# Kernel optimization log

Hardware: AMD Instinct MI355X
Metric: run time of the kernel (lower is better)

The kernel has to match this reference:

```python
import jax, jax.numpy as jnp
import numpy as np

N_NODES = 100000
N_EDGES = 1600000
N_GRAPHS = 64
D = 128          # input_features == hidden_sf*model_dim == out_sf*output_channels
N_CLASSES = 10   # out_dim
N_LAYERS = 3


def setup_inputs() -> dict:
    key = jax.random.key(0)
    ks = jax.random.split(key, 8)
    x = jax.random.normal(ks[0], (N_NODES, D), dtype=jnp.float32)
    edge_index = jax.random.randint(ks[1], (2, N_EDGES), 0, N_NODES, dtype=jnp.int64)
    batch = jnp.sort(jax.random.randint(ks[2], (N_NODES,), 0, N_GRAPHS, dtype=jnp.int64))
    s = 1.0 / np.sqrt(D)
    # PyG GraphConv: out = lin_rel(aggr(x_j)) + lin_root(x); lin_root has no bias
    W_rel = jax.random.uniform(ks[3], (N_LAYERS, D, D), jnp.float32, -s, s)
    W_root = jax.random.uniform(ks[4], (N_LAYERS, D, D), jnp.float32, -s, s)
    b_rel = jax.random.uniform(ks[5], (N_LAYERS, D), jnp.float32, -s, s)
    W_fc = jax.random.uniform(ks[6], (D, N_CLASSES), jnp.float32, -s, s)
    b_fc = jax.random.uniform(ks[7], (N_CLASSES,), jnp.float32, -s, s)
    return dict(x=x, edge_index=edge_index, batch=batch,
                W_rel=W_rel, W_root=W_root, b_rel=b_rel, W_fc=W_fc, b_fc=b_fc)


def reference(x, edge_index, batch, W_rel, W_root, b_rel, W_fc, b_fc):
    src, dst = edge_index[0], edge_index[1]  # messages flow src -> dst
    for i in range(N_LAYERS):  # small fixed layer count
        agg = jax.ops.segment_sum(x[src], dst, num_segments=N_NODES)  # [N, D] gather+scatter-add
        x = agg @ W_rel[i] + b_rel[i] + x @ W_root[i]
    # global mean pool over graphs
    counts = jax.ops.segment_sum(jnp.ones((N_NODES,), x.dtype), batch, num_segments=N_GRAPHS)
    pooled = jax.ops.segment_sum(x, batch, num_segments=N_GRAPHS) / jnp.maximum(counts, 1.0)[:, None]
    logits = pooled @ W_fc + b_fc  # [N_GRAPHS, N_CLASSES]
    return jax.nn.log_softmax(logits, axis=1)
```

## Files before the change

### kernel.cpp

```cpp
#include <hip/hip_runtime.h>
#include <hip/hip_bf16.h>

#define D 128
#define NGRAPHS 64
#define NCLASSES 10
#define NB 800
#define CAP 3072
#define EPB 8192

typedef unsigned short u16;
typedef unsigned int u32;
typedef __attribute__((ext_vector_type(8))) short bf16x8;
typedef __attribute__((ext_vector_type(4))) float f32x4;

__device__ __forceinline__ u16 rne_bf16(float f) {
  u32 u = __float_as_uint(f);
  u += 0x7FFFu + ((u >> 16) & 1u);
  return (u16)(u >> 16);
}
__device__ __forceinline__ float bf_lo(u32 u) { return __uint_as_float(u << 16); }
__device__ __forceinline__ float bf_hi(u32 u) { return __uint_as_float(u & 0xFFFF0000u); }

__device__ __forceinline__ void gload_lds16(const void* g, void* l) {
  __builtin_amdgcn_global_load_lds(
      (const __attribute__((address_space(1))) void*)g,
      (__attribute__((address_space(3))) void*)l, 16, 0, 0);
}

__global__ __launch_bounds__(256) void k_cast0(const float* __restrict__ x,
                                               u16* __restrict__ xb, long long n8) {
  long long i = (long long)blockIdx.x * 256 + threadIdx.x;
  if (i >= n8) return;
  const float4* xp = reinterpret_cast<const float4*>(x) + i * 2;
  float4 a = xp[0], b = xp[1];
  u32 w0 = rne_bf16(a.x) | ((u32)rne_bf16(a.y) << 16);
  u32 w1 = rne_bf16(a.z) | ((u32)rne_bf16(a.w) << 16);
  u32 w2 = rne_bf16(b.x) | ((u32)rne_bf16(b.y) << 16);
  u32 w3 = rne_bf16(b.z) | ((u32)rne_bf16(b.w) << 16);
  reinterpret_cast<uint4*>(xb)[i] = make_uint4(w0, w1, w2, w3);
}

__global__ __launch_bounds__(256) void k_prep_wt(const float* __restrict__ W_rel,
                                                 const float* __restrict__ W_root,
                                                 u16* __restrict__ Wt) {
  int id = blockIdx.x * 256 + threadIdx.x;
  if (id >= 6 * D * D) return;
  int col = id & 127;
  int k = (id >> 7) & 127;
  int m = id >> 14;
  const float* src = (m < 3) ? (W_rel + (size_t)m * D * D) : (W_root + (size_t)(m - 3) * D * D);
  Wt[(size_t)m * D * D + col * D + k] = rne_bf16(src[k * D + col]);
}

__global__ __launch_bounds__(256) void k_bin(
    const int* __restrict__ src, const int* __restrict__ dst,
    int* __restrict__ gcnt, u32* __restrict__ ebuf, int n_edges, int nb) {
  __shared__ int lh[NB];
  int tid = threadIdx.x;
  int e0 = blockIdx.x * EPB;
  for (int b = tid; b < NB; b += 256) lh[b] = 0;
  __syncthreads();
  for (int i = tid; i < EPB; i += 256) {
    int e = e0 + i;
    if (e < n_edges) atomicAdd(&lh[dst[e] >> 7], 1);
  }
  __syncthreads();
  for (int b = tid; b < nb; b += 256) {
    int c = lh[b];
    lh[b] = (c > 0) ? (b * CAP + atomicAdd(&gcnt[b], c)) : 0;
  }
  __syncthreads();
  for (int i = tid; i < EPB; i += 256) {
    int e = e0 + i;
    if (e < n_edges) {
      int d = dst[e];
      int slot = atomicAdd(&lh[d >> 7], 1);
      ebuf[slot] = ((u32)(d & 127) << 20) | (u32)src[e];
    }
  }
}

__global__ __launch_bounds__(256) void k_sort(
    const u32* __restrict__ ebuf, const int* __restrict__ gcnt,
    u32* __restrict__ eidx, int* __restrict__ rowptr, int* __restrict__ deg,
    int n_nodes) {
  __shared__ u32 earr[CAP];
  __shared__ int lh[128], sc[128], lcur[128];
  int tid = threadIdx.x;
  int b = blockIdx.x;
  int cnt = gcnt[b];
  int base = b * CAP;
  for (int i = tid; i < cnt; i += 256) earr[i] = ebuf[base + i];
  if (tid < 128) lh[tid] = 0;
  __syncthreads();
  for (int i = tid; i < cnt; i += 256) atomicAdd(&lh[earr[i] >> 20], 1);
  __syncthreads();
  if (tid < 128) sc[tid] = lh[tid];
  __syncthreads();
  #pragma unroll
  for (int off = 1; off < 128; off <<= 1) {
    int v = (tid < 128 && tid >= off) ? sc[tid - off] : 0;
    __syncthreads();
    if (tid < 128) sc[tid] += v;
    __syncthreads();
  }
  if (tid < 128) {
    int excl = sc[tid] - lh[tid];
    int n = b * 128 + tid;
    if (n < n_nodes) { rowptr[n] = base + excl; deg[n] = lh[tid]; }
    lcur[tid] = excl;
  }
  __syncthreads();
  for (int i = tid; i < cnt; i += 256) {
    u32 e = earr[i];
    int slot = atomicAdd(&lcur[e >> 20], 1);
    eidx[base + slot] = e & 0xFFFFF;
  }
}

__global__ __launch_bounds__(256) void k_gather(
    const u16* __restrict__ xb, const int* __restrict__ rowptr,
    const int* __restrict__ deg, const u32* __restrict__ eidx,
    u16* __restrict__ aggb, int n_nodes) {
  int tid = threadIdx.x;
  int lane = tid & 63;
  int n = blockIdx.x * 4 + (tid >> 6);
  if (n >= n_nodes) return;
  int es = lane >> 4;
  int c = lane & 15;
  int beg = rowptr[n];
  int dn = deg[n];
  float a0 = 0, a1 = 0, a2 = 0, a3 = 0, a4 = 0, a5 = 0, a6 = 0, a7 = 0;
  int i = 0;
  for (; i + 8 <= dn; i += 8) {
    int s0 = (int)eidx[beg + i + es];
    int s1 = (int)eidx[beg + i + 4 + es];
    uint4 v0 = *(reinterpret_cast<const uint4*>(xb + (size_t)s0 * D) + c);
    uint4 v1 = *(reinterpret_cast<const uint4*>(xb + (size_t)s1 * D) + c);
    a0 += bf_lo(v0.x) + bf_lo(v1.x); a1 += bf_hi(v0.x) + bf_hi(v1.x);
    a2 += bf_lo(v0.y) + bf_lo(v1.y); a3 += bf_hi(v0.y) + bf_hi(v1.y);
    a4 += bf_lo(v0.z) + bf_lo(v1.z); a5 += bf_hi(v0.z) + bf_hi(v1.z);
    a6 += bf_lo(v0.w) + bf_lo(v1.w); a7 += bf_hi(v0.w) + bf_hi(v1.w);
  }
  for (; i < dn; i += 4) {
    bool p = (i + es) < dn;
    int s = p ? (int)eidx[beg + i + es] : 0;
    if (p) {
      uint4 v = *(reinterpret_cast<const uint4*>(xb + (size_t)s * D) + c);
      a0 += bf_lo(v.x); a1 += bf_hi(v.x);
      a2 += bf_lo(v.y); a3 += bf_hi(v.y);
      a4 += bf_lo(v.z); a5 += bf_hi(v.z);
      a6 += bf_lo(v.w); a7 += bf_hi(v.w);
    }
  }
  #pragma unroll
  for (int d = 16; d <= 32; d <<= 1) {
    a0 += __shfl_xor(a0, d); a1 += __shfl_xor(a1, d);
    a2 += __shfl_xor(a2, d); a3 += __shfl_xor(a3, d);
    a4 += __shfl_xor(a4, d); a5 += __shfl_xor(a5, d);
    a6 += __shfl_xor(a6, d); a7 += __shfl_xor(a7, d);
  }
  if (es == 0) {
    u32 w0 = rne_bf16(a0) | ((u32)rne_bf16(a1) << 16);
    u32 w1 = rne_bf16(a2) | ((u32)rne_bf16(a3) << 16);
    u32 w2 = rne_bf16(a4) | ((u32)rne_bf16(a5) << 16);
    u32 w3 = rne_bf16(a6) | ((u32)rne_bf16(a7) << 16);
    *(reinterpret_cast<uint4*>(aggb + (size_t)n * D) + c) = make_uint4(w0, w1, w2, w3);
  }
}

__global__ __launch_bounds__(256) void k_gemm_mfma(
    const u16* __restrict__ A1, const u16* __restrict__ A2,
    const u16* __restrict__ Wt1, const u16* __restrict__ Wt2,
    const float* __restrict__ bias, u16* __restrict__ outp, int M) {
  __shared__ __align__(16) u16 As[2][128 * 64];
  __shared__ __align__(16) u16 Ws[2][128 * 64];
  int tid = threadIdx.x;
  int wave = tid >> 6, lane = tid & 63;
  int g = lane >> 4, lr = lane & 15;
  int r0 = blockIdx.x * 128;
  int wr = wave * 32;

  f32x4 acc[2][8];
  #pragma unroll
  for (int fr = 0; fr < 2; fr++)
    #pragma unroll
    for (int fc = 0; fc < 8; fc++)
      acc[fr][fc] = (f32x4){0.f, 0.f, 0.f, 0.f};

  const u16* Am[2] = {A1, A2};
  const u16* Wm[2] = {Wt1, Wt2};

  auto STAGE = [&](int buf, const u16* A, const u16* Wt, int kh) {
    #pragma unroll
    for (int i = 0; i < 4; i++) {
      int gI = i * 256 + tid;
      int row = gI >> 3;
      int cs = (gI & 7) ^ (row & 7);
      int rg = r0 + row; if (rg >= M) rg = M - 1;
      u16* la = &As[buf][(size_t)(i * 256 + wave * 64) * 8];
      gload_lds16(A + (size_t)rg * D + kh * 64 + cs * 8, la);
      u16* lw = &Ws[buf][(size_t)(i * 256 + wave * 64) * 8];
      gload_lds16(Wt + (size_t)row * D + kh * 64 + cs * 8, lw);
    }
  };

  STAGE(0, A1, Wt1, 0);
  __syncthreads();

  #pragma unroll 1
  for (int s = 0; s < 4; s++) {
    if (s < 3) {
      int ns = s + 1;
      STAGE(ns & 1, Am[ns >> 1], Wm[ns >> 1], ns & 1);
    }
    int buf = s & 1;
    #pragma unroll
    for (int kc = 0; kc < 2; kc++) {
      int kbyte = kc * 64 + g * 16;
      bf16x8 af[2];
      #pragma unroll
      for (int fr = 0; fr < 2; fr++) {
        int row = wr + fr * 16 + lr;
        int ob = (kbyte ^ ((row & 7) << 4)) >> 1;
        af[fr] = *reinterpret_cast<const bf16x8*>(&As[buf][row * 64 + ob]);
      }
      #pragma unroll
      for (int fc = 0; fc < 8; fc++) {
        int colw = fc * 16 + lr;
        int ob = (kbyte ^ ((colw & 7) << 4)) >> 1;
        bf16x8 bfv = *reinterpret_cast<const bf16x8*>(&Ws[buf][colw * 64 + ob]);
        #pragma unroll
        for (int fr = 0; fr < 2; fr++)
          acc[fr][fc] = __builtin_amdgcn_mfma_f32_16x16x32_bf16(
              af[fr], bfv, acc[fr][fc], 0, 0, 0);
      }
    }
    __syncthreads();
  }

  #pragma unroll
  for (int fc = 0; fc < 8; fc++) {
    float bc = bias[fc * 16 + lr];
    #pragma unroll
    for (int fr = 0; fr < 2; fr++) {
      #pragma unroll
      for (int j = 0; j < 4; j++) {
        int R = r0 + wr + fr * 16 + g * 4 + j;
        if (R < M)
          outp[(size_t)R * D + fc * 16 + lr] = rne_bf16(acc[fr][fc][j] + bc);
      }
    }
  }
}

#define CHUNK 256
__global__ __launch_bounds__(256) void k_pool(
    const u16* __restrict__ xb, const int* __restrict__ batch,
    float* __restrict__ pooled, int n_nodes) {
  int col = threadIdx.x & 127;
  int sub = threadIdx.x >> 7;
  int n0 = blockIdx.x * CHUNK;
  int nend = min(n0 + CHUNK, n_nodes);
  float sum = 0.f; int cur = -1;
  for (int n = n0 + sub; n < nend; n += 2) {
    int g = batch[n];
    if (g != cur) {
      if (cur >= 0) atomicAdd(&pooled[cur * D + col], sum);
      sum = 0.f; cur = g;
    }
    sum += __uint_as_float((u32)xb[(size_t)n * D + col] << 16);
  }
  if (cur >= 0) atomicAdd(&pooled[cur * D + col], sum);
}

__global__ __launch_bounds__(256) void k_bounds(
    const int* __restrict__ batch, int* __restrict__ start, int n) {
  int i = blockIdx.x * 256 + threadIdx.x;
  if (i >= n) return;
  int g = batch[i];
  if (i == 0 || batch[i - 1] != g) start[g] = i;
}

__global__ void k_head(const float* __restrict__ pooled, const int* __restrict__ gstart,
                       const float* __restrict__ W_fc, const float* __restrict__ b_fc,
                       float* __restrict__ outp, int n_nodes) {
  int g = threadIdx.x;
  if (g >= NGRAPHS) return;
  int s = gstart[g];
  int c = 0;
  if (s >= 0) {
    int e = n_nodes;
    for (int h = g + 1; h < NGRAPHS; h++)
      if (gstart[h] >= 0) { e = gstart[h]; break; }
    c = e - s;
  }
  float inv = 1.0f / fmaxf((float)c, 1.0f);
  float logits[NCLASSES];
  #pragma unroll
  for (int j = 0; j < NCLASSES; j++) logits[j] = b_fc[j];
  for (int k = 0; k < D; k++) {
    float p = pooled[g * D + k] * inv;
    #pragma unroll
    for (int j = 0; j < NCLASSES; j++) logits[j] += p * W_fc[k * NCLASSES + j];
  }
  float m = logits[0];
  #pragma unroll
  for (int j = 1; j < NCLASSES; j++) m = fmaxf(m, logits[j]);
  float s2 = 0.f;
  #pragma unroll
  for (int j = 0; j < NCLASSES; j++) s2 += expf(logits[j] - m);
  float lse = m + logf(s2);
  #pragma unroll
  for (int j = 0; j < NCLASSES; j++) outp[g * NCLASSES + j] = logits[j] - lse;
}

extern "C" void kernel_launch(void* const* d_in, const int* in_sizes, int n_in,
                              void* d_out, int out_size, void* d_ws, size_t ws_size,
                              hipStream_t stream) {
  const float* x      = (const float*)d_in[0];
  const int*   ei     = (const int*)d_in[1];
  const int*   batch  = (const int*)d_in[2];
  const float* W_rel  = (const float*)d_in[3];
  const float* W_root = (const float*)d_in[4];
  const float* b_rel  = (const float*)d_in[5];
  const float* W_fc   = (const float*)d_in[6];
  const float* b_fc   = (const float*)d_in[7];
  float* outp = (float*)d_out;

  int n_nodes = in_sizes[0] / D;
  int n_edges = in_sizes[1] / 2;
  const int* src = ei;
  const int* dst = ei + n_edges;
  int nb = (n_nodes + 127) / 128;

  char* ws = (char*)d_ws;
  size_t bb = (size_t)n_nodes * D * sizeof(u16);
  size_t nbts = (size_t)n_nodes * sizeof(int);
  u16* aggb   = (u16*)(ws);
  u16* xba    = (u16*)(ws + bb);
  u16* xbb    = (u16*)(ws + 2 * bb);
  char* p     = ws + 3 * bb;
  u16* Wt     = (u16*)(p);               p += (size_t)6 * D * D * sizeof(u16);
  int* gcnt   = (int*)(p);               p += (size_t)NB * sizeof(int);
  u32* ebuf   = (u32*)(p);               p += (size_t)NB * CAP * sizeof(u32);
  u32* eidx   = (u32*)(p);               p += (size_t)NB * CAP * sizeof(u32);
  int* rowptr = (int*)(p);               p += nbts;
  int* deg    = (int*)(p);               p += nbts;
  float* pooled = (float*)(p);           p += (size_t)NGRAPHS * D * sizeof(float);
  int* gstart = (int*)(p);

  k_prep_wt<<<(6 * D * D + 255) / 256, 256, 0, stream>>>(W_rel, W_root, Wt);
  long long n8 = (long long)n_nodes * D / 8;
  k_cast0<<<(int)((n8 + 255) / 256), 256, 0, stream>>>(x, xba, n8);
  hipMemsetAsync(gcnt, 0, (size_t)NB * sizeof(int), stream);
  k_bin<<<(n_edges + EPB - 1) / EPB, 256, 0, stream>>>(src, dst, gcnt, ebuf, n_edges, nb);
  k_sort<<<nb, 256, 0, stream>>>(ebuf, gcnt, eidx, rowptr, deg, n_nodes);

  u16* xc = xba;
  u16* xn = xbb;
  int gemmblk = (n_nodes + 127) / 128;
  for (int l = 0; l < 3; l++) {
    k_gather<<<(n_nodes + 3) / 4, 256, 0, stream>>>(xc, rowptr, deg, eidx, aggb, n_nodes);
    k_gemm_mfma<<<gemmblk, 256, 0, stream>>>(
        aggb, xc, Wt + (size_t)l * D * D, Wt + (size_t)(3 + l) * D * D,
        b_rel + (size_t)l * D, xn, n_nodes);
    u16* t = xc; xc = xn; xn = t;
  }

  hipMemsetAsync(pooled, 0, (size_t)NGRAPHS * D * sizeof(float), stream);
  hipMemsetAsync(gstart, 0xFF, (size_t)NGRAPHS * sizeof(int), stream);
  k_pool<<<(n_nodes + CHUNK - 1) / CHUNK, 256, 0, stream>>>(xc, batch, pooled, n_nodes);
  k_bounds<<<(n_nodes + 255) / 256, 256, 0, stream>>>(batch, gstart, n_nodes);
  k_head<<<1, 64, 0, stream>>>(pooled, gstart, W_fc, b_fc, outp, n_nodes);
}
```

Measured before the change: 486.2 us.

## Fuse mean-pool, graph bounds and classifier head into one per-graph kernel

Replaces the atomic pooling kernel, the graph-bounds kernel, the head kernel and two memsets with one kernel that launches one block per graph. Each block binary-searches the sorted batch array for its node range, sums rows with vectorized loads and a shared-memory tree reduction, then computes logits and log-softmax. This removes launches, memsets and atomics. The cost is that only 64 blocks stream the whole feature matrix, which may limit bandwidth and leaves it sensitive to uneven graph sizes.

Result: faster. 468.2 us (-3.7%).

```diff
diff --git a/kernel.cpp b/kernel.cpp
--- a/kernel.cpp
+++ b/kernel.cpp
@@ -254,65 +254,72 @@
   }
 }
 
-#define CHUNK 256
-__global__ __launch_bounds__(256) void k_pool(
+__global__ __launch_bounds__(256) void k_poolhead(
     const u16* __restrict__ xb, const int* __restrict__ batch,
-    float* __restrict__ pooled, int n_nodes) {
-  int col = threadIdx.x & 127;
-  int sub = threadIdx.x >> 7;
-  int n0 = blockIdx.x * CHUNK;
-  int nend = min(n0 + CHUNK, n_nodes);
-  float sum = 0.f; int cur = -1;
-  for (int n = n0 + sub; n < nend; n += 2) {
-    int g = batch[n];
-    if (g != cur) {
-      if (cur >= 0) atomicAdd(&pooled[cur * D + col], sum);
-      sum = 0.f; cur = g;
-    }
-    sum += __uint_as_float((u32)xb[(size_t)n * D + col] << 16);
-  }
-  if (cur >= 0) atomicAdd(&pooled[cur * D + col], sum);
-}
-
-__global__ __launch_bounds__(256) void k_bounds(
-    const int* __restrict__ batch, int* __restrict__ start, int n) {
-  int i = blockIdx.x * 256 + threadIdx.x;
-  if (i >= n) return;
-  int g = batch[i];
-  if (i == 0 || batch[i - 1] != g) start[g] = i;
-}
-
-__global__ void k_head(const float* __restrict__ pooled, const int* __restrict__ gstart,
-                       const float* __restrict__ W_fc, const float* __restrict__ b_fc,
-                       float* __restrict__ outp, int n_nodes) {
-  int g = threadIdx.x;
-  if (g >= NGRAPHS) return;
-  int s = gstart[g];
-  int c = 0;
-  if (s >= 0) {
-    int e = n_nodes;
-    for (int h = g + 1; h < NGRAPHS; h++)
-      if (gstart[h] >= 0) { e = gstart[h]; break; }
-    c = e - s;
-  }
-  float inv = 1.0f / fmaxf((float)c, 1.0f);
-  float logits[NCLASSES];
-  #pragma unroll
-  for (int j = 0; j < NCLASSES; j++) logits[j] = b_fc[j];
-  for (int k = 0; k < D; k++) {
-    float p = pooled[g * D + k] * inv;
-    #pragma unroll
-    for (int j = 0; j < NCLASSES; j++) logits[j] += p * W_fc[k * NCLASSES + j];
-  }
-  float m = logits[0];
-  #pragma unroll
-  for (int j = 1; j < NCLASSES; j++) m = fmaxf(m, logits[j]);
-  float s2 = 0.f;
-  #pragma unroll
-  for (int j = 0; j < NCLASSES; j++) s2 += expf(logits[j] - m);
-  float lse = m + logf(s2);
-  #pragma unroll
-  for (int j = 0; j < NCLASSES; j++) outp[g * NCLASSES + j] = logits[j] - lse;
+    const float* __restrict__ W_fc, const float* __restrict__ b_fc,
+    float* __restrict__ outp, int n_nodes) {
+  __shared__ float pp[16][128];
+  __shared__ float lg[128][NCLASSES];
+  int tid = threadIdx.x;
+  int g = blockIdx.x;
+  int rs = tid >> 4, c = tid & 15;
+
+  int lo = 0, hi = n_nodes;
+  while (lo < hi) { int m = (lo + hi) >> 1; if (batch[m] < g) lo = m + 1; else hi = m; }
+  int start = lo;
+  hi = n_nodes;
+  while (lo < hi) { int m = (lo + hi) >> 1; if (batch[m] < g + 1) lo = m + 1; else hi = m; }
+  int end = lo;
+  int cnt = end - start;
+
+  float a0 = 0, a1 = 0, a2 = 0, a3 = 0, a4 = 0, a5 = 0, a6 = 0, a7 = 0;
+  for (int r = start + rs; r < end; r += 16) {
+    uint4 v = *(reinterpret_cast<const uint4*>(xb + (size_t)r * D) + c);
+    a0 += bf_lo(v.x); a1 += bf_hi(v.x);
+    a2 += bf_lo(v.y); a3 += bf_hi(v.y);
+    a4 += bf_lo(v.z); a5 += bf_hi(v.z);
+    a6 += bf_lo(v.w); a7 += bf_hi(v.w);
+  }
+  pp[rs][c * 8 + 0] = a0; pp[rs][c * 8 + 1] = a1;
+  pp[rs][c * 8 + 2] = a2; pp[rs][c * 8 + 3] = a3;
+  pp[rs][c * 8 + 4] = a4; pp[rs][c * 8 + 5] = a5;
+  pp[rs][c * 8 + 6] = a6; pp[rs][c * 8 + 7] = a7;
+  __syncthreads();
+  for (int s = 8; s >= 1; s >>= 1) {
+    if (rs < s) {
+      #pragma unroll
+      for (int j = 0; j < 8; j++) pp[rs][c * 8 + j] += pp[rs + s][c * 8 + j];
+    }
+    __syncthreads();
+  }
+  float inv = 1.0f / fmaxf((float)cnt, 1.0f);
+  if (tid < 128) {
+    float p = pp[0][tid] * inv;
+    #pragma unroll
+    for (int j = 0; j < NCLASSES; j++) lg[tid][j] = p * W_fc[tid * NCLASSES + j];
+  }
+  __syncthreads();
+  for (int s = 64; s >= 1; s >>= 1) {
+    if (tid < s) {
+      #pragma unroll
+      for (int j = 0; j < NCLASSES; j++) lg[tid][j] += lg[tid + s][j];
+    }
+    __syncthreads();
+  }
+  if (tid == 0) {
+    float logits[NCLASSES];
+    #pragma unroll
+    for (int j = 0; j < NCLASSES; j++) logits[j] = lg[0][j] + b_fc[j];
+    float m = logits[0];
+    #pragma unroll
+    for (int j = 1; j < NCLASSES; j++) m = fmaxf(m, logits[j]);
+    float s2 = 0.f;
+    #pragma unroll
+    for (int j = 0; j < NCLASSES; j++) s2 += expf(logits[j] - m);
+    float lse = m + logf(s2);
+    #pragma unroll
+    for (int j = 0; j < NCLASSES; j++) outp[g * NCLASSES + j] = logits[j] - lse;
+  }
 }
 
 extern "C" void kernel_launch(void* const* d_in, const int* in_sizes, int n_in,
@@ -347,8 +354,6 @@
   u32* eidx   = (u32*)(p);               p += (size_t)NB * CAP * sizeof(u32);
   int* rowptr = (int*)(p);               p += nbts;
   int* deg    = (int*)(p);               p += nbts;
-  float* pooled = (float*)(p);           p += (size_t)NGRAPHS * D * sizeof(float);
-  int* gstart = (int*)(p);
 
   k_prep_wt<<<(6 * D * D + 255) / 256, 256, 0, stream>>>(W_rel, W_root, Wt);
   long long n8 = (long long)n_nodes * D / 8;
@@ -368,9 +373,5 @@
     u16* t = xc; xc = xn; xn = t;
   }
 
-  hipMemsetAsync(pooled, 0, (size_t)NGRAPHS * D * sizeof(float), stream);
-  hipMemsetAsync(gstart, 0xFF, (size_t)NGRAPHS * sizeof(int), stream);
-  k_pool<<<(n_nodes + CHUNK - 1) / CHUNK, 256, 0, stream>>>(xc, batch, pooled, n_nodes);
-  k_bounds<<<(n_nodes + 255) / 256, 256, 0, stream>>>(batch, gstart, n_nodes);
-  k_head<<<1, 64, 0, stream>>>(pooled, gstart, W_fc, b_fc, outp, n_nodes);
-}
+  k_poolhead<<<NGRAPHS, 256, 0, stream>>>(xc, batch, W_fc, b_fc, outp, n_nodes);
+}
```
